# Optimization experiments

Hardware: AMD Instinct MI355X
Metric: run time of the kernel (lower is better)

## Reference

```python
import jax, jax.numpy as jnp
import numpy as np

DIM = 1024
HEADS = 16
DIM_HEAD = 64
B, N = 4, 2048


def setup_inputs() -> dict:
    key = jax.random.key(0)
    ks = jax.random.split(key, 10)
    s = 0.02
    x = jax.random.normal(ks[0], (B, N, DIM), dtype=jnp.float32)
    Wq = jax.random.normal(ks[1], (DIM, DIM), dtype=jnp.float32) * s
    bq = jnp.zeros((DIM,), dtype=jnp.float32)
    Wk = jax.random.normal(ks[2], (DIM, DIM), dtype=jnp.float32) * s
    bk = jnp.zeros((DIM,), dtype=jnp.float32)
    Wv = jax.random.normal(ks[3], (DIM, DIM), dtype=jnp.float32) * s
    bv = jnp.zeros((DIM,), dtype=jnp.float32)
    Wo = jax.random.normal(ks[4], (DIM, DIM), dtype=jnp.float32) * s
    bo = jnp.zeros((DIM,), dtype=jnp.float32)
    # learnable log-temperature, init = log(dim_head ** -0.5)
    log_temp = jnp.array(np.log(DIM_HEAD ** -0.5), dtype=jnp.float32)
    return {"x": x, "Wq": Wq, "bq": bq, "Wk": Wk, "bk": bk,
            "Wv": Wv, "bv": bv, "Wo": Wo, "bo": bo, "log_temp": log_temp}


def reference(x, Wq, bq, Wk, bk, Wv, bv, Wo, bo, log_temp):
    b, n, _ = x.shape
    # projections (dropout is identity at p=0)
    q = x @ Wq + bq
    k = x @ Wk + bk
    v = x @ Wv + bv
    # [b, n, h*d] -> [b, h, n, d]
    def split_heads(t):
        return t.reshape(b, n, HEADS, DIM_HEAD).transpose(0, 2, 1, 3)
    q, k, v = split_heads(q), split_heads(k), split_heads(v)
    # scaled dot-product scores with learnable temperature
    dots = jnp.einsum('bhid,bhjd->bhij', q, k) * jnp.exp(log_temp)
    # mask out self-attention (diagonal) with -finfo.max
    mask_value = -jnp.finfo(dots.dtype).max
    eye = jnp.eye(n, dtype=bool)
    dots = jnp.where(eye, mask_value, dots)
    attn = jax.nn.softmax(dots, axis=-1)
    out = jnp.einsum('bhij,bhjd->bhid', attn, v)
    # [b, h, n, d] -> [b, n, h*d]
    out = out.transpose(0, 2, 1, 3).reshape(b, n, HEADS * DIM_HEAD)
    return out @ Wo + bo
```

## Files before the change

kernel.cpp:

```cpp
#include <hip/hip_runtime.h>
#include <cmath>

typedef __bf16 bf16_t;
typedef __attribute__((ext_vector_type(8))) __bf16 bf16x8;
typedef __attribute__((ext_vector_type(4))) __bf16 bf16x4;
typedef __attribute__((ext_vector_type(2))) __bf16 bf16x2;
typedef __attribute__((ext_vector_type(4))) float f32x4;
typedef __attribute__((ext_vector_type(4))) unsigned uint4v;

#define SEQ   2048
#define NHEAD 16
#define DHEAD 64
#define NB    4
#define DIMSZ 1024
#define MROWS 8192

__device__ __forceinline__ void async_copy16(const void* g, void* lds) {
  __builtin_amdgcn_global_load_lds(
      (__attribute__((address_space(1))) void*)(g),
      (__attribute__((address_space(3))) void*)(lds), 16, 0, 0);
}

__device__ __forceinline__ f32x4 f32x4_zero() {
  f32x4 v; v[0] = 0.f; v[1] = 0.f; v[2] = 0.f; v[3] = 0.f; return v;
}

__device__ __forceinline__ void permlane_xform(unsigned& a, unsigned& b) {
#if __has_builtin(__builtin_amdgcn_permlane32_swap) && __has_builtin(__builtin_amdgcn_permlane16_swap)
  typedef __attribute__((ext_vector_type(2))) unsigned uint2v;
  uint2v r1 = __builtin_amdgcn_permlane32_swap(a, b, false, false);
  uint2v r2 = __builtin_amdgcn_permlane16_swap(r1[0], r1[1], false, false);
  a = r2[0]; b = r2[1];
#else
  asm volatile("v_permlane32_swap_b32 %0, %1\n\t"
               "v_permlane16_swap_b32 %0, %1"
               : "+v"(a), "+v"(b));
#endif
}

__device__ __forceinline__ unsigned pack_bf16(float lo, float hi) {
  bf16x2 t; t[0] = (__bf16)lo; t[1] = (__bf16)hi;
  return __builtin_bit_cast(unsigned, t);
}

__global__ __launch_bounds__(256) void cvt_x(const float* __restrict__ x,
                                             bf16_t* __restrict__ xb) {
  size_t i = ((size_t)blockIdx.x * 256 + threadIdx.x) * 8;
  float4 f0 = *(const float4*)(x + i);
  float4 f1 = *(const float4*)(x + i + 4);
  bf16x8 o;
  o[0] = (__bf16)f0.x; o[1] = (__bf16)f0.y; o[2] = (__bf16)f0.z; o[3] = (__bf16)f0.w;
  o[4] = (__bf16)f1.x; o[5] = (__bf16)f1.y; o[6] = (__bf16)f1.z; o[7] = (__bf16)f1.w;
  *(bf16x8*)(xb + i) = o;
}

__global__ __launch_bounds__(256) void transpose_w(
    const float* __restrict__ W0, const float* __restrict__ W1,
    const float* __restrict__ W2, const float* __restrict__ W3,
    bf16_t* __restrict__ T0, bf16_t* __restrict__ T1,
    bf16_t* __restrict__ T2, bf16_t* __restrict__ T3) {
  const float* W; bf16_t* T;
  switch (blockIdx.z) {
    case 0: W = W0; T = T0; break;
    case 1: W = W1; T = T1; break;
    case 2: W = W2; T = T2; break;
    default: W = W3; T = T3; break;
  }
  __shared__ float t[32][33];
  int tx = threadIdx.x, ty = threadIdx.y;
  int col = blockIdx.x * 32 + tx;
#pragma unroll
  for (int i = 0; i < 4; i++) {
    int row = blockIdx.y * 32 + ty + i * 8;
    t[ty + i * 8][tx] = W[row * DIMSZ + col];
  }
  __syncthreads();
#pragma unroll
  for (int i = 0; i < 4; i++) {
    int n = blockIdx.x * 32 + ty + i * 8;
    int k = blockIdx.y * 32 + tx;
    T[n * DIMSZ + k] = (bf16_t)t[tx][ty + i * 8];
  }
}

__device__ __forceinline__ void gemm_mainloop(
    const bf16_t* __restrict__ A, const bf16_t* __restrict__ Bt,
    int m0, int n0, f32x4 acc[4][4]) {
  __shared__ __attribute__((aligned(16))) bf16_t As[2][128 * 64];
  __shared__ __attribute__((aligned(16))) bf16_t Bs[2][128 * 64];
  const int tid = threadIdx.x;
  const int wid = tid >> 6, lane = tid & 63;
  const int quad = lane >> 4, l16 = lane & 15;
  const int wm = wid & 1, wn = wid >> 1;
  const int srow = lane >> 3;
  const int gchunk = (lane & 7) ^ srow;
#pragma unroll
  for (int r = 0; r < 4; r++)
#pragma unroll
    for (int c = 0; c < 4; c++) acc[r][c] = f32x4_zero();

  const bf16_t* ag = A + (size_t)(m0 + wid * 8 + srow) * DIMSZ + gchunk * 8;
  const bf16_t* bg = Bt + (size_t)(n0 + wid * 8 + srow) * DIMSZ + gchunk * 8;

  auto stage = [&](int k0, int buf) {
#pragma unroll
    for (int c2 = 0; c2 < 4; c2++) {
      async_copy16(ag + (size_t)c2 * 32 * DIMSZ + k0, &As[buf][(c2 * 32 + wid * 8) * 64]);
      async_copy16(bg + (size_t)c2 * 32 * DIMSZ + k0, &Bs[buf][(c2 * 32 + wid * 8) * 64]);
    }
  };

  stage(0, 0);
  for (int it = 0; it < 16; it++) {
    const int p = it & 1;
    __syncthreads();
    if (it < 15) stage((it + 1) * 64, 1 - p);
#pragma unroll
    for (int kk = 0; kk < 2; kk++) {
      bf16x8 af[4], bfr[4];
#pragma unroll
      for (int r = 0; r < 4; r++) {
        int row = wm * 64 + r * 16 + l16;
        int slot = (kk * 4 + quad) ^ (row & 7);
        af[r] = *(const bf16x8*)(&As[p][0] + row * 64 + slot * 8);
      }
#pragma unroll
      for (int c = 0; c < 4; c++) {
        int row = wn * 64 + c * 16 + l16;
        int slot = (kk * 4 + quad) ^ (row & 7);
        bfr[c] = *(const bf16x8*)(&Bs[p][0] + row * 64 + slot * 8);
      }
#pragma unroll
      for (int r = 0; r < 4; r++)
#pragma unroll
        for (int c = 0; c < 4; c++)
          acc[r][c] = __builtin_amdgcn_mfma_f32_16x16x32_bf16(af[r], bfr[c],
                                                              acc[r][c], 0, 0, 0);
    }
  }
}

__global__ __launch_bounds__(256, 2) void gemm_qkv(
    const bf16_t* __restrict__ A,
    const bf16_t* __restrict__ Wt0, const bf16_t* __restrict__ Wt1,
    const bf16_t* __restrict__ Wt2,
    const float* __restrict__ b0, const float* __restrict__ b1,
    const float* __restrict__ b2,
    bf16_t* __restrict__ o0, bf16_t* __restrict__ o1, bf16_t* __restrict__ o2) {
  const bf16_t* Bt; const float* bias; bf16_t* dst;
  if (blockIdx.z == 0)      { Bt = Wt0; bias = b0; dst = o0; }
  else if (blockIdx.z == 1) { Bt = Wt1; bias = b1; dst = o1; }
  else                      { Bt = Wt2; bias = b2; dst = o2; }
  const int m0 = blockIdx.x * 128, n0 = blockIdx.y * 128;
  f32x4 acc[4][4];
  gemm_mainloop(A, Bt, m0, n0, acc);
  const int lane = threadIdx.x & 63, wid = threadIdx.x >> 6;
  const int quad = lane >> 4, l16 = lane & 15;
  const int wm = wid & 1, wn = wid >> 1;
  if (blockIdx.z == 2) {
#pragma unroll
    for (int c = 0; c < 4; c++) {
      int col = n0 + wn * 64 + c * 16 + l16;
      float bv = bias[col];
      int hh = col >> 6, dd = col & 63;
#pragma unroll
      for (int r = 0; r < 4; r++) {
        int row = m0 + wm * 64 + r * 16 + quad * 4;
        int bb = row >> 11, nn = row & (SEQ - 1);
        bf16x4 pk;
#pragma unroll
        for (int rr = 0; rr < 4; rr++) pk[rr] = (__bf16)(acc[r][c][rr] + bv);
        *(bf16x4*)(dst + ((size_t)(bb * NHEAD + hh) * DHEAD + dd) * SEQ + nn) = pk;
      }
    }
  } else {
#pragma unroll
    for (int c = 0; c < 4; c++) {
      int col = n0 + wn * 64 + c * 16 + l16;
      float bv = bias[col];
      int hh = col >> 6, dd = col & 63;
#pragma unroll
      for (int r = 0; r < 4; r++)
#pragma unroll
        for (int rr = 0; rr < 4; rr++) {
          int row = m0 + wm * 64 + r * 16 + quad * 4 + rr;
          int bb = row >> 11, nn = row & (SEQ - 1);
          dst[(((size_t)(bb * NHEAD + hh) * SEQ + nn) << 6) + dd] =
              (bf16_t)(acc[r][c][rr] + bv);
        }
    }
  }
}

__global__ __launch_bounds__(256, 2) void gemm_out(
    const bf16_t* __restrict__ A, const bf16_t* __restrict__ Bt,
    const float* __restrict__ bias, float* __restrict__ dst) {
  const int m0 = blockIdx.x * 128, n0 = blockIdx.y * 128;
  f32x4 acc[4][4];
  gemm_mainloop(A, Bt, m0, n0, acc);
  const int lane = threadIdx.x & 63, wid = threadIdx.x >> 6;
  const int quad = lane >> 4, l16 = lane & 15;
  const int wm = wid & 1, wn = wid >> 1;
#pragma unroll
  for (int c = 0; c < 4; c++) {
    int col = n0 + wn * 64 + c * 16 + l16;
    float bv = bias[col];
#pragma unroll
    for (int r = 0; r < 4; r++)
#pragma unroll
      for (int rr = 0; rr < 4; rr++) {
        int row = m0 + wm * 64 + r * 16 + quad * 4 + rr;
        dst[(size_t)row * DIMSZ + col] = acc[r][c][rr] + bv;
      }
  }
}

__global__ __launch_bounds__(256, 4) void attn_kernel(
    const bf16_t* __restrict__ qh, const bf16_t* __restrict__ kh,
    const bf16_t* __restrict__ vt, bf16_t* __restrict__ ao,
    const float* __restrict__ log_temp) {
  __shared__ __attribute__((aligned(16))) bf16_t Ks[2][64 * 64];
  __shared__ __attribute__((aligned(16))) bf16_t Vs[2][64 * 64];
  const int tid = threadIdx.x;
  const int wid = tid >> 6, lane = tid & 63;
  const int quad = lane >> 4, l16 = lane & 15;
  const int f = blockIdx.x;
  const int hb = f & 63;
  const int h = hb & 15, b = hb >> 4;
  const int i0 = (f >> 6) * 128;
  const size_t ho = (size_t)(b * NHEAD + h) * SEQ * DHEAD;
  const bf16_t* Q = qh + ho;
  const float ascale = expf(log_temp[0]) * 1.44269504f;
  const float bshift = 16.0f * 1.44269504f;

  const int irow = i0 + wid * 32;
  bf16x8 qf[2][2];
#pragma unroll
  for (int g = 0; g < 2; g++)
#pragma unroll
    for (int jj = 0; jj < 2; jj++)
      qf[g][jj] = *(const bf16x8*)(Q + (size_t)(irow + g * 16 + l16) * DHEAD +
                                   jj * 32 + quad * 8);

  f32x4 oaccT[4][2];
#pragma unroll
  for (int c = 0; c < 4; c++)
#pragma unroll
    for (int g = 0; g < 2; g++) oaccT[c][g] = f32x4_zero();
  float lsum[2] = {0.f, 0.f};

  const int srow = lane >> 3;
  const int gch = (lane & 7) ^ srow;
  const bf16_t* kg = kh + ho + (size_t)(wid * 8 + srow) * DHEAD + gch * 8;
  const bf16_t* vg = vt + ho + (size_t)(wid * 8 + srow) * SEQ + gch * 8;
  const int x7 = l16 & 7;
  const int jdiag_t = (f >> 6) * 2 + (wid >> 1);

  int kvoff[4][2];
#pragma unroll
  for (int c = 0; c < 4; c++)
#pragma unroll
    for (int kk = 0; kk < 2; kk++)
      kvoff[c][kk] = (c * 16 + l16) * 64 + (((kk * 4) + quad) ^ x7) * 8;

  auto stage = [&](int jt, int buf) {
    const bf16_t* kp = kg + (size_t)jt * 64 * DHEAD;
    const bf16_t* vp = vg + jt * 64;
    bf16_t* kd = &Ks[buf][wid * 8 * 64];
    bf16_t* vd = &Vs[buf][wid * 8 * 64];
    async_copy16(kp, kd);
    async_copy16(kp + 32 * DHEAD, kd + 32 * 64);
    async_copy16(vp, vd);
    async_copy16(vp + 32 * SEQ, vd + 32 * 64);
  };

  stage(0, 0);
  for (int jt = 0; jt < SEQ / 64; jt++) {
    const int p = jt & 1;
    __syncthreads();
    if (jt + 1 < SEQ / 64) stage(jt + 1, 1 - p);
    const bf16_t* Kp = &Ks[p][0];
    const bf16_t* Vp = &Vs[p][0];

    f32x4 st[4][2];
#pragma unroll
    for (int c = 0; c < 4; c++) {
      bf16x8 kf0 = *(const bf16x8*)(Kp + kvoff[c][0]);
      bf16x8 kf1 = *(const bf16x8*)(Kp + kvoff[c][1]);
#pragma unroll
      for (int g = 0; g < 2; g++) {
        f32x4 s = f32x4_zero();
        s = __builtin_amdgcn_mfma_f32_16x16x32_bf16(kf0, qf[g][0], s, 0, 0, 0);
        s = __builtin_amdgcn_mfma_f32_16x16x32_bf16(kf1, qf[g][1], s, 0, 0, 0);
        st[c][g] = s;
      }
    }

    const int j0 = jt * 64;
    unsigned pkv[2][4][2];
    if (jt == jdiag_t) {
#pragma unroll
      for (int g = 0; g < 2; g++) {
        float ls = 0.f;
        const int ig = irow + g * 16 + l16;
#pragma unroll
        for (int c = 0; c < 4; c++) {
          float e[4];
#pragma unroll
          for (int rr = 0; rr < 4; rr++) {
            float v = __builtin_amdgcn_exp2f(fmaf(st[c][g][rr], ascale, -bshift));
            if (j0 + c * 16 + quad * 4 + rr == ig) v = 0.f;
            e[rr] = v;
          }
          ls += (e[0] + e[1]) + (e[2] + e[3]);
          pkv[g][c][0] = pack_bf16(e[0], e[1]);
          pkv[g][c][1] = pack_bf16(e[2], e[3]);
        }
        lsum[g] += ls;
      }
    } else {
#pragma unroll
      for (int g = 0; g < 2; g++) {
        float ls = 0.f;
#pragma unroll
        for (int c = 0; c < 4; c++) {
          float e[4];
#pragma unroll
          for (int rr = 0; rr < 4; rr++)
            e[rr] = __builtin_amdgcn_exp2f(fmaf(st[c][g][rr], ascale, -bshift));
          ls += (e[0] + e[1]) + (e[2] + e[3]);
          pkv[g][c][0] = pack_bf16(e[0], e[1]);
          pkv[g][c][1] = pack_bf16(e[2], e[3]);
        }
        lsum[g] += ls;
      }
    }

    bf16x8 pb[2][2];
#pragma unroll
    for (int g = 0; g < 2; g++) {
#pragma unroll
      for (int kk = 0; kk < 2; kk++) {
        unsigned a0 = pkv[g][2 * kk][0], b0 = pkv[g][2 * kk + 1][0];
        unsigned a1 = pkv[g][2 * kk][1], b1 = pkv[g][2 * kk + 1][1];
        permlane_xform(a0, b0);
        permlane_xform(a1, b1);
        uint4v u = {a0, a1, b0, b1};
        pb[g][kk] = __builtin_bit_cast(bf16x8, u);
      }
    }

#pragma unroll
    for (int c = 0; c < 4; c++) {
      bf16x8 va0 = *(const bf16x8*)(Vp + kvoff[c][0]);
      bf16x8 va1 = *(const bf16x8*)(Vp + kvoff[c][1]);
#pragma unroll
      for (int g = 0; g < 2; g++) {
        oaccT[c][g] = __builtin_amdgcn_mfma_f32_16x16x32_bf16(va0, pb[g][0],
                                                              oaccT[c][g], 0, 0, 0);
        oaccT[c][g] = __builtin_amdgcn_mfma_f32_16x16x32_bf16(va1, pb[g][1],
                                                              oaccT[c][g], 0, 0, 0);
      }
    }
  }

#pragma unroll
  for (int g = 0; g < 2; g++) {
    lsum[g] += __shfl_xor(lsum[g], 16);
    lsum[g] += __shfl_xor(lsum[g], 32);
    lsum[g] = 1.f / lsum[g];
  }
#pragma unroll
  for (int g = 0; g < 2; g++) {
    const int row = irow + g * 16 + l16;
#pragma unroll
    for (int c = 0; c < 4; c++) {
      bf16x4 o;
#pragma unroll
      for (int rr = 0; rr < 4; rr++) o[rr] = (__bf16)(oaccT[c][g][rr] * lsum[g]);
      *(bf16x4*)(ao + (size_t)(b * SEQ + row) * DIMSZ + h * DHEAD + c * 16 +
                 quad * 4) = o;
    }
  }
}

extern "C" void kernel_launch(void* const* d_in, const int* in_sizes, int n_in,
                              void* d_out, int out_size, void* d_ws, size_t ws_size,
                              hipStream_t stream) {
  const float* x  = (const float*)d_in[0];
  const float* Wq = (const float*)d_in[1];
  const float* bq = (const float*)d_in[2];
  const float* Wk = (const float*)d_in[3];
  const float* bk = (const float*)d_in[4];
  const float* Wv = (const float*)d_in[5];
  const float* bv = (const float*)d_in[6];
  const float* Wo = (const float*)d_in[7];
  const float* bo = (const float*)d_in[8];
  const float* lt = (const float*)d_in[9];

  bf16_t* xb  = (bf16_t*)d_ws;
  bf16_t* wtq = xb  + (size_t)MROWS * DIMSZ;
  bf16_t* wtk = wtq + (size_t)DIMSZ * DIMSZ;
  bf16_t* wtv = wtk + (size_t)DIMSZ * DIMSZ;
  bf16_t* wto = wtv + (size_t)DIMSZ * DIMSZ;
  bf16_t* qh  = wto + (size_t)DIMSZ * DIMSZ;
  bf16_t* kh  = qh  + (size_t)MROWS * DIMSZ;
  bf16_t* vh  = kh  + (size_t)MROWS * DIMSZ;
  bf16_t* ao  = xb;

  cvt_x<<<dim3(MROWS * DIMSZ / 2048), dim3(256), 0, stream>>>(x, xb);
  transpose_w<<<dim3(32, 32, 4), dim3(32, 8), 0, stream>>>(
      Wq, Wk, Wv, Wo, wtq, wtk, wtv, wto);
  gemm_qkv<<<dim3(64, 8, 3), dim3(256), 0, stream>>>(
      xb, wtq, wtk, wtv, bq, bk, bv, qh, kh, vh);
  attn_kernel<<<dim3(16 * NHEAD * NB), dim3(256), 0, stream>>>(qh, kh, vh, ao, lt);
  gemm_out<<<dim3(64, 8), dim3(256), 0, stream>>>(ao, wto, bo, (float*)d_out);
}
```

Baseline: 269.6 us.

## Switch attention to fp16 with prescaled Q and MFMA row-sum

```diff
diff --git a/kernel.cpp b/kernel.cpp
--- a/kernel.cpp
+++ b/kernel.cpp
@@ -2,9 +2,12 @@
 #include <cmath>
 
 typedef __bf16 bf16_t;
+typedef _Float16 f16_t;
 typedef __attribute__((ext_vector_type(8))) __bf16 bf16x8;
 typedef __attribute__((ext_vector_type(4))) __bf16 bf16x4;
-typedef __attribute__((ext_vector_type(2))) __bf16 bf16x2;
+typedef __attribute__((ext_vector_type(8))) _Float16 f16x8;
+typedef __attribute__((ext_vector_type(4))) _Float16 f16x4;
+typedef __attribute__((ext_vector_type(2))) __fp16 fp16x2n;
 typedef __attribute__((ext_vector_type(4))) float f32x4;
 typedef __attribute__((ext_vector_type(4))) unsigned uint4v;
 
@@ -38,9 +41,9 @@
 #endif
 }
 
-__device__ __forceinline__ unsigned pack_bf16(float lo, float hi) {
-  bf16x2 t; t[0] = (__bf16)lo; t[1] = (__bf16)hi;
-  return __builtin_bit_cast(unsigned, t);
+__device__ __forceinline__ unsigned pkrtz(float a, float b) {
+  fp16x2n r = __builtin_amdgcn_cvt_pkrtz(a, b);
+  return __builtin_bit_cast(unsigned, r);
 }
 
 __global__ __launch_bounds__(256) void cvt_x(const float* __restrict__ x,
@@ -111,6 +114,7 @@
   };
 
   stage(0, 0);
+#pragma unroll 2
   for (int it = 0; it < 16; it++) {
     const int p = it & 1;
     __syncthreads();
@@ -146,8 +150,8 @@
     const bf16_t* __restrict__ Wt2,
     const float* __restrict__ b0, const float* __restrict__ b1,
     const float* __restrict__ b2,
-    bf16_t* __restrict__ o0, bf16_t* __restrict__ o1, bf16_t* __restrict__ o2) {
-  const bf16_t* Bt; const float* bias; bf16_t* dst;
+    f16_t* __restrict__ o0, f16_t* __restrict__ o1, f16_t* __restrict__ o2) {
+  const bf16_t* Bt; const float* bias; f16_t* dst;
   if (blockIdx.z == 0)      { Bt = Wt0; bias = b0; dst = o0; }
   else if (blockIdx.z == 1) { Bt = Wt1; bias = b1; dst = o1; }
   else                      { Bt = Wt2; bias = b2; dst = o2; }
@@ -167,10 +171,10 @@
       for (int r = 0; r < 4; r++) {
         int row = m0 + wm * 64 + r * 16 + quad * 4;
         int bb = row >> 11, nn = row & (SEQ - 1);
-        bf16x4 pk;
-#pragma unroll
-        for (int rr = 0; rr < 4; rr++) pk[rr] = (__bf16)(acc[r][c][rr] + bv);
-        *(bf16x4*)(dst + ((size_t)(bb * NHEAD + hh) * DHEAD + dd) * SEQ + nn) = pk;
+        f16x4 pk;
+#pragma unroll
+        for (int rr = 0; rr < 4; rr++) pk[rr] = (f16_t)(acc[r][c][rr] + bv);
+        *(f16x4*)(dst + ((size_t)(bb * NHEAD + hh) * DHEAD + dd) * SEQ + nn) = pk;
       }
     }
   } else {
@@ -186,7 +190,7 @@
           int row = m0 + wm * 64 + r * 16 + quad * 4 + rr;
           int bb = row >> 11, nn = row & (SEQ - 1);
           dst[(((size_t)(bb * NHEAD + hh) * SEQ + nn) << 6) + dd] =
-              (bf16_t)(acc[r][c][rr] + bv);
+              (f16_t)(acc[r][c][rr] + bv);
         }
     }
   }
@@ -216,11 +220,11 @@
 }
 
 __global__ __launch_bounds__(256, 4) void attn_kernel(
-    const bf16_t* __restrict__ qh, const bf16_t* __restrict__ kh,
-    const bf16_t* __restrict__ vt, bf16_t* __restrict__ ao,
+    const f16_t* __restrict__ qh, const f16_t* __restrict__ kh,
+    const f16_t* __restrict__ vt, bf16_t* __restrict__ ao,
     const float* __restrict__ log_temp) {
-  __shared__ __attribute__((aligned(16))) bf16_t Ks[2][64 * 64];
-  __shared__ __attribute__((aligned(16))) bf16_t Vs[2][64 * 64];
+  __shared__ __attribute__((aligned(16))) f16_t Ks[2][64 * 64];
+  __shared__ __attribute__((aligned(16))) f16_t Vs[2][64 * 64];
   const int tid = threadIdx.x;
   const int wid = tid >> 6, lane = tid & 63;
   const int quad = lane >> 4, l16 = lane & 15;
@@ -229,30 +233,36 @@
   const int h = hb & 15, b = hb >> 4;
   const int i0 = (f >> 6) * 128;
   const size_t ho = (size_t)(b * NHEAD + h) * SEQ * DHEAD;
-  const bf16_t* Q = qh + ho;
-  const float ascale = expf(log_temp[0]) * 1.44269504f;
-  const float bshift = 16.0f * 1.44269504f;
+  const f16_t* Q = qh + ho;
+  const float qscale = expf(log_temp[0]) * 1.44269504f;
 
   const int irow = i0 + wid * 32;
-  bf16x8 qf[2][2];
+  f16x8 qf[2][2];
 #pragma unroll
   for (int g = 0; g < 2; g++)
 #pragma unroll
-    for (int jj = 0; jj < 2; jj++)
-      qf[g][jj] = *(const bf16x8*)(Q + (size_t)(irow + g * 16 + l16) * DHEAD +
-                                   jj * 32 + quad * 8);
+    for (int jj = 0; jj < 2; jj++) {
+      f16x8 raw = *(const f16x8*)(Q + (size_t)(irow + g * 16 + l16) * DHEAD +
+                                  jj * 32 + quad * 8);
+#pragma unroll
+      for (int e = 0; e < 8; e++) qf[g][jj][e] = (f16_t)((float)raw[e] * qscale);
+    }
+  f16x8 ones;
+#pragma unroll
+  for (int e = 0; e < 8; e++) ones[e] = (f16_t)1.0f;
 
   f32x4 oaccT[4][2];
 #pragma unroll
   for (int c = 0; c < 4; c++)
 #pragma unroll
     for (int g = 0; g < 2; g++) oaccT[c][g] = f32x4_zero();
-  float lsum[2] = {0.f, 0.f};
+  f32x4 acc_l[2];
+  acc_l[0] = f32x4_zero(); acc_l[1] = f32x4_zero();
 
   const int srow = lane >> 3;
   const int gch = (lane & 7) ^ srow;
-  const bf16_t* kg = kh + ho + (size_t)(wid * 8 + srow) * DHEAD + gch * 8;
-  const bf16_t* vg = vt + ho + (size_t)(wid * 8 + srow) * SEQ + gch * 8;
+  const f16_t* kg = kh + ho + (size_t)(wid * 8 + srow) * DHEAD + gch * 8;
+  const f16_t* vg = vt + ho + (size_t)(wid * 8 + srow) * SEQ + gch * 8;
   const int x7 = l16 & 7;
   const int jdiag_t = (f >> 6) * 2 + (wid >> 1);
 
@@ -264,10 +274,10 @@
       kvoff[c][kk] = (c * 16 + l16) * 64 + (((kk * 4) + quad) ^ x7) * 8;
 
   auto stage = [&](int jt, int buf) {
-    const bf16_t* kp = kg + (size_t)jt * 64 * DHEAD;
-    const bf16_t* vp = vg + jt * 64;
-    bf16_t* kd = &Ks[buf][wid * 8 * 64];
-    bf16_t* vd = &Vs[buf][wid * 8 * 64];
+    const f16_t* kp = kg + (size_t)jt * 64 * DHEAD;
+    const f16_t* vp = vg + jt * 64;
+    f16_t* kd = &Ks[buf][wid * 8 * 64];
+    f16_t* vd = &Vs[buf][wid * 8 * 64];
     async_copy16(kp, kd);
     async_copy16(kp + 32 * DHEAD, kd + 32 * 64);
     async_copy16(vp, vd);
@@ -275,23 +285,24 @@
   };
 
   stage(0, 0);
+#pragma unroll 2
   for (int jt = 0; jt < SEQ / 64; jt++) {
     const int p = jt & 1;
     __syncthreads();
     if (jt + 1 < SEQ / 64) stage(jt + 1, 1 - p);
-    const bf16_t* Kp = &Ks[p][0];
-    const bf16_t* Vp = &Vs[p][0];
+    const f16_t* Kp = &Ks[p][0];
+    const f16_t* Vp = &Vs[p][0];
 
     f32x4 st[4][2];
 #pragma unroll
     for (int c = 0; c < 4; c++) {
-      bf16x8 kf0 = *(const bf16x8*)(Kp + kvoff[c][0]);
-      bf16x8 kf1 = *(const bf16x8*)(Kp + kvoff[c][1]);
+      f16x8 kf0 = *(const f16x8*)(Kp + kvoff[c][0]);
+      f16x8 kf1 = *(const f16x8*)(Kp + kvoff[c][1]);
 #pragma unroll
       for (int g = 0; g < 2; g++) {
         f32x4 s = f32x4_zero();
-        s = __builtin_amdgcn_mfma_f32_16x16x32_bf16(kf0, qf[g][0], s, 0, 0, 0);
-        s = __builtin_amdgcn_mfma_f32_16x16x32_bf16(kf1, qf[g][1], s, 0, 0, 0);
+        s = __builtin_amdgcn_mfma_f32_16x16x32_f16(kf0, qf[g][0], s, 0, 0, 0);
+        s = __builtin_amdgcn_mfma_f32_16x16x32_f16(kf1, qf[g][1], s, 0, 0, 0);
         st[c][g] = s;
       }
     }
@@ -301,44 +312,35 @@
     if (jt == jdiag_t) {
 #pragma unroll
       for (int g = 0; g < 2; g++) {
-        float ls = 0.f;
         const int ig = irow + g * 16 + l16;
 #pragma unroll
         for (int c = 0; c < 4; c++) {
           float e[4];
 #pragma unroll
           for (int rr = 0; rr < 4; rr++) {
-            float v = __builtin_amdgcn_exp2f(fmaf(st[c][g][rr], ascale, -bshift));
+            float v = __builtin_amdgcn_exp2f(st[c][g][rr]);
             if (j0 + c * 16 + quad * 4 + rr == ig) v = 0.f;
             e[rr] = v;
           }
-          ls += (e[0] + e[1]) + (e[2] + e[3]);
-          pkv[g][c][0] = pack_bf16(e[0], e[1]);
-          pkv[g][c][1] = pack_bf16(e[2], e[3]);
+          pkv[g][c][0] = pkrtz(e[0], e[1]);
+          pkv[g][c][1] = pkrtz(e[2], e[3]);
         }
-        lsum[g] += ls;
       }
     } else {
 #pragma unroll
-      for (int g = 0; g < 2; g++) {
-        float ls = 0.f;
+      for (int g = 0; g < 2; g++)
 #pragma unroll
         for (int c = 0; c < 4; c++) {
-          float e[4];
-#pragma unroll
-          for (int rr = 0; rr < 4; rr++)
-            e[rr] = __builtin_amdgcn_exp2f(fmaf(st[c][g][rr], ascale, -bshift));
-          ls += (e[0] + e[1]) + (e[2] + e[3]);
-          pkv[g][c][0] = pack_bf16(e[0], e[1]);
-          pkv[g][c][1] = pack_bf16(e[2], e[3]);
+          pkv[g][c][0] = pkrtz(__builtin_amdgcn_exp2f(st[c][g][0]),
+                               __builtin_amdgcn_exp2f(st[c][g][1]));
+          pkv[g][c][1] = pkrtz(__builtin_amdgcn_exp2f(st[c][g][2]),
+                               __builtin_amdgcn_exp2f(st[c][g][3]));
         }
-        lsum[g] += ls;
-      }
-    }
-
-    bf16x8 pb[2][2];
-#pragma unroll
-    for (int g = 0; g < 2; g++) {
+    }
+
+    f16x8 pb[2][2];
+#pragma unroll
+    for (int g = 0; g < 2; g++)
 #pragma unroll
       for (int kk = 0; kk < 2; kk++) {
         unsigned a0 = pkv[g][2 * kk][0], b0 = pkv[g][2 * kk + 1][0];
@@ -346,30 +348,32 @@
         permlane_xform(a0, b0);
         permlane_xform(a1, b1);
         uint4v u = {a0, a1, b0, b1};
-        pb[g][kk] = __builtin_bit_cast(bf16x8, u);
-      }
+        pb[g][kk] = __builtin_bit_cast(f16x8, u);
+      }
+
+#pragma unroll
+    for (int g = 0; g < 2; g++) {
+      acc_l[g] = __builtin_amdgcn_mfma_f32_16x16x32_f16(ones, pb[g][0], acc_l[g], 0, 0, 0);
+      acc_l[g] = __builtin_amdgcn_mfma_f32_16x16x32_f16(ones, pb[g][1], acc_l[g], 0, 0, 0);
     }
 
 #pragma unroll
     for (int c = 0; c < 4; c++) {
-      bf16x8 va0 = *(const bf16x8*)(Vp + kvoff[c][0]);
-      bf16x8 va1 = *(const bf16x8*)(Vp + kvoff[c][1]);
+      f16x8 va0 = *(const f16x8*)(Vp + kvoff[c][0]);
+      f16x8 va1 = *(const f16x8*)(Vp + kvoff[c][1]);
 #pragma unroll
       for (int g = 0; g < 2; g++) {
-        oaccT[c][g] = __builtin_amdgcn_mfma_f32_16x16x32_bf16(va0, pb[g][0],
-                                                              oaccT[c][g], 0, 0, 0);
-        oaccT[c][g] = __builtin_amdgcn_mfma_f32_16x16x32_bf16(va1, pb[g][1],
-                                                              oaccT[c][g], 0, 0, 0);
-      }
-    }
-  }
-
-#pragma unroll
-  for (int g = 0; g < 2; g++) {
-    lsum[g] += __shfl_xor(lsum[g], 16);
-    lsum[g] += __shfl_xor(lsum[g], 32);
-    lsum[g] = 1.f / lsum[g];
-  }
+        oaccT[c][g] = __builtin_amdgcn_mfma_f32_16x16x32_f16(va0, pb[g][0],
+                                                             oaccT[c][g], 0, 0, 0);
+        oaccT[c][g] = __builtin_amdgcn_mfma_f32_16x16x32_f16(va1, pb[g][1],
+                                                             oaccT[c][g], 0, 0, 0);
+      }
+    }
+  }
+
+  float inv[2];
+  inv[0] = 1.f / acc_l[0][0];
+  inv[1] = 1.f / acc_l[1][0];
 #pragma unroll
   for (int g = 0; g < 2; g++) {
     const int row = irow + g * 16 + l16;
@@ -377,7 +381,7 @@
     for (int c = 0; c < 4; c++) {
       bf16x4 o;
 #pragma unroll
-      for (int rr = 0; rr < 4; rr++) o[rr] = (__bf16)(oaccT[c][g][rr] * lsum[g]);
+      for (int rr = 0; rr < 4; rr++) o[rr] = (__bf16)(oaccT[c][g][rr] * inv[g]);
       *(bf16x4*)(ao + (size_t)(b * SEQ + row) * DIMSZ + h * DHEAD + c * 16 +
                  quad * 4) = o;
     }
@@ -403,9 +407,9 @@
   bf16_t* wtk = wtq + (size_t)DIMSZ * DIMSZ;
   bf16_t* wtv = wtk + (size_t)DIMSZ * DIMSZ;
   bf16_t* wto = wtv + (size_t)DIMSZ * DIMSZ;
-  bf16_t* qh  = wto + (size_t)DIMSZ * DIMSZ;
-  bf16_t* kh  = qh  + (size_t)MROWS * DIMSZ;
-  bf16_t* vh  = kh  + (size_t)MROWS * DIMSZ;
+  f16_t*  qh  = (f16_t*)(wto + (size_t)DIMSZ * DIMSZ);
+  f16_t*  kh  = qh  + (size_t)MROWS * DIMSZ;
+  f16_t*  vh  = kh  + (size_t)MROWS * DIMSZ;
   bf16_t* ao  = xb;
 
   cvt_x<<<dim3(MROWS * DIMSZ / 2048), dim3(256), 0, stream>>>(x, xb);
```

New measurement: 258.6 us. 1.04x faster.
